# Kernel tuning notes

Hardware: AMD Instinct MI355X
Metric: run time of the kernel (lower is better)

Reference implementation:

```python
import jax, jax.numpy as jnp
import numpy as np

N, K, E = 20000, 4, 320000
IN_DIM, H_IN, D = 1024, 256, 128
GATE_IN = 2 * D + 1  # [h || m || logdeg]
GATE_H = 128         # max(d_out, 32)
TEMP = 0.6
M_CLAMP = 20.0


def _init(key, shape, fan_in):
    return jax.random.normal(key, shape, dtype=jnp.float32) / np.sqrt(fan_in)


def setup_inputs() -> dict:
    key = jax.random.key(0)
    ks = jax.random.split(key, 24)
    inp = {}
    inp['X'] = jax.random.normal(ks[0], (N, IN_DIM), dtype=jnp.float32)
    inp['rows'] = jax.random.randint(ks[1], (K, E), 0, N, dtype=jnp.int32)
    inp['cols'] = jax.random.randint(ks[2], (K, E), 0, N, dtype=jnp.int32)
    inp['mask'] = jnp.ones((N, K), dtype=jnp.float32)
    inp['logdeg'] = jax.random.uniform(ks[3], (N, K), dtype=jnp.float32) * 3.0
    # lin_in: 3-layer MLP 1024 -> 256 -> 256 -> 128, each + ReLU
    inp['W_in0'] = _init(ks[4], (IN_DIM, H_IN), IN_DIM); inp['b_in0'] = jnp.zeros((H_IN,), jnp.float32)
    inp['W_in1'] = _init(ks[5], (H_IN, H_IN), H_IN);     inp['b_in1'] = jnp.zeros((H_IN,), jnp.float32)
    inp['W_in2'] = _init(ks[6], (H_IN, D), H_IN);        inp['b_in2'] = jnp.zeros((D,), jnp.float32)
    # block 0
    inp['Wmsg0'] = _init(ks[7], (D, D), D)
    inp['Wg1_0'] = _init(ks[8], (GATE_IN, GATE_H), GATE_IN); inp['bg1_0'] = jnp.zeros((GATE_H,), jnp.float32)
    inp['Wg2_0'] = _init(ks[9], (GATE_H, 1), GATE_H);        inp['bg2_0'] = jnp.zeros((1,), jnp.float32)
    # block 1
    inp['Wmsg1'] = _init(ks[10], (D, D), D)
    inp['Wg1_1'] = _init(ks[11], (GATE_IN, GATE_H), GATE_IN); inp['bg1_1'] = jnp.zeros((GATE_H,), jnp.float32)
    inp['Wg2_1'] = _init(ks[12], (GATE_H, 1), GATE_H);        inp['bg2_1'] = jnp.zeros((1,), jnp.float32)
    # head
    inp['Wh1'] = _init(ks[13], (D, D), D); inp['bh1'] = jnp.zeros((D,), jnp.float32)
    inp['Wh2'] = _init(ks[14], (D, 1), D); inp['bh2'] = jnp.zeros((1,), jnp.float32)
    return inp


def reference(X, rows, cols, mask, logdeg,
              W_in0, b_in0, W_in1, b_in1, W_in2, b_in2,
              Wmsg0, Wg1_0, bg1_0, Wg2_0, bg2_0,
              Wmsg1, Wg1_1, bg1_1, Wg2_1, bg2_1,
              Wh1, bh1, Wh2, bh2):
    relu = jax.nn.relu
    # input encoder (eval mode: dropout / featdrop are identity)
    H = relu(relu(relu(X @ W_in0 + b_in0) @ W_in1 + b_in1) @ W_in2 + b_in2)

    def pairnorm(x):
        x = x - x.mean(axis=0, keepdims=True)
        mean_norm = jnp.sqrt(jnp.mean(jnp.sum(x * x, axis=1))) + 1e-6
        return x / mean_norm

    def block(H, Wmsg, Wg1, bg1, Wg2, bg2):
        Z = H @ Wmsg  # [N, D]
        def prop(r, c):  # sparse A_k @ Z with binary adjacency: out[r] += Z[c]
            return jax.ops.segment_sum(Z[c], r, num_segments=N)
        M = jnp.transpose(jax.vmap(prop)(rows, cols), (1, 0, 2))  # [N, K, D]
        M = jnp.clip(M, -M_CLAMP, M_CLAMP)
        H_rep = jnp.broadcast_to(H[:, None, :], (N, K, H.shape[1]))
        gate_in = jnp.concatenate([H_rep, M, logdeg[:, :, None]], axis=2)  # [N, K, 2D+1]
        scores = (relu(gate_in @ Wg1 + bg1) @ Wg2 + bg2)[..., 0]  # [N, K]
        alpha = jax.nn.softmax(scores / TEMP, axis=1)
        alpha = alpha * mask
        alpha = alpha / jnp.maximum(alpha.sum(axis=1, keepdims=True), 1e-12)
        alpha = jnp.maximum(alpha, 1e-8)
        alpha = alpha / jnp.maximum(alpha.sum(axis=1, keepdims=True), 1e-12)
        fused = jnp.einsum('nk,nkd->nd', alpha, M)
        return fused, alpha

    fused0, a0 = block(H, Wmsg0, Wg1_0, bg1_0, Wg2_0, bg2_0)
    H = relu(pairnorm(fused0 + H))
    fused1, a1 = block(H, Wmsg1, Wg1_1, bg1_1, Wg2_1, bg2_1)
    H = relu(pairnorm(fused1 + H))

    h = relu(relu(H) @ Wh1 + bh1)
    logits = (h @ Wh2 + bh2)[:, 0]  # [N]
    return logits, jnp.stack([a0, a1], axis=0)
```

## Files before the change

### kernel.cpp

```cpp
#include <hip/hip_runtime.h>
#include <hip/hip_bf16.h>

#define N_NODES 20000
#define KADJ 4
#define NEDGE 320000
#define ETOTAL (KADJ * NEDGE)
#define IN_DIM_ 1024
#define H_IN_ 256
#define DDIM 128
#define GATE_H_ 128
#define TEMP_ 0.6f
#define M_CLAMP_ 20.0f
#define CSR_TOTAL (KADJ * N_NODES)
#define NCOARSE 128
#define QPER (CSR_TOTAL / NCOARSE)
#define ESTRIDE 12288
#define TILE_A 4096
#define BINA_NB ((ETOTAL + TILE_A - 1) / TILE_A)
#define NB_CAST (N_NODES * IN_DIM_ / 8 / 256)
#define NB_TRANS 2560

typedef __attribute__((ext_vector_type(8))) short frag_ab;
typedef __attribute__((ext_vector_type(4))) float frag_cd;
typedef __attribute__((ext_vector_type(8))) unsigned short us8;

__device__ inline unsigned short f2bf(float f) {
    unsigned int u = __float_as_uint(f);
    u += 0x7FFFu + ((u >> 16) & 1);
    return (unsigned short)(u >> 16);
}
__device__ inline float bflo(unsigned int p) { return __uint_as_float(p << 16); }
__device__ inline float bfhi(unsigned int p) { return __uint_as_float(p & 0xffff0000u); }

__device__ __forceinline__ void gld16(const unsigned short* g, unsigned short* l) {
    __builtin_amdgcn_global_load_lds(
        (const __attribute__((address_space(1))) void*)g,
        (__attribute__((address_space(3))) void*)l, 16, 0, 0);
}

#define PIPE_WAIT_NEXT()  asm volatile("s_waitcnt vmcnt(5)" ::: "memory")
#define PIPE_WAIT_LAST()  asm volatile("s_waitcnt vmcnt(0)" ::: "memory")
#define PIPE_BAR()        __builtin_amdgcn_s_barrier()
#define PIPE_FENCE()      __builtin_amdgcn_sched_barrier(0)


struct TD { const float* src; unsigned short* dst; int K; int N; };
struct TD10 { TD d[10]; };

__global__ __launch_bounds__(256) void prep_kernel(
    const float* __restrict__ X, unsigned short* __restrict__ Xb,
    TD10 descs,
    const int* __restrict__ rows, const int* __restrict__ cols,
    int* __restrict__ bcnt, uint2* __restrict__ staging)
{
    __shared__ __align__(16) char sraw[2048 + TILE_A * 8];
    int bid = blockIdx.x;
    int tid = threadIdx.x;

    if (bid >= BINA_NB + NB_TRANS) {
        int i = ((bid - BINA_NB - NB_TRANS) * 256 + tid) * 8;
        float4 a = *(const float4*)(X + i), b = *(const float4*)(X + i + 4);
        us8 o;
        o[0] = f2bf(a.x); o[1] = f2bf(a.y); o[2] = f2bf(a.z); o[3] = f2bf(a.w);
        o[4] = f2bf(b.x); o[5] = f2bf(b.y); o[6] = f2bf(b.z); o[7] = f2bf(b.w);
        *(us8*)(Xb + i) = o;
        return;
    }
    if (bid >= BINA_NB) {
        int b2 = bid - BINA_NB;
        TD t = descs.d[b2 >> 8];
        int rem = b2 & 255;
        int n0 = (rem & 7) * 32, k0 = (rem >> 3) * 32;
        if (n0 >= t.N || k0 >= t.K) return;
        float (*tile)[33] = (float(*)[33])sraw;
        int tx = tid & 31, ty4 = (tid >> 5) * 4;
#pragma unroll
        for (int i = 0; i < 4; i++)
            tile[ty4 + i][tx] = t.src[(size_t)(k0 + ty4 + i) * t.N + n0 + tx];
        __syncthreads();
#pragma unroll
        for (int i = 0; i < 4; i++)
            t.dst[(size_t)(n0 + ty4 + i) * t.K + k0 + tx] = f2bf(tile[tx][ty4 + i]);
        return;
    }
    int* hist  = (int*)sraw;
    int* hscan = hist + NCOARSE;
    int* lcur  = hscan + NCOARSE;
    int* gbase = lcur + NCOARSE;
    uint2* pairs = (uint2*)(sraw + 2048);

    int base = bid * TILE_A;
    int cnt_t = min(TILE_A, ETOTAL - base);

    for (int i = tid; i < NCOARSE; i += 256) hist[i] = 0;
    __syncthreads();

    unsigned int q[16], c[16];
    bool valid[16];
#pragma unroll
    for (int i = 0; i < 16; i++) {
        int loc = i * 256 + tid;
        valid[i] = loc < cnt_t;
        if (valid[i]) {
            int e = base + loc;
            int k = e / NEDGE;
            unsigned int qq = (unsigned int)(k * N_NODES + rows[e]);
            q[i] = qq;
            c[i] = (unsigned int)cols[e];
            atomicAdd(&hist[qq / QPER], 1);
        }
    }
    __syncthreads();
    if (tid < NCOARSE) hscan[tid] = hist[tid];
    __syncthreads();
    for (int d = 1; d < NCOARSE; d <<= 1) {
        int v = (tid >= d && tid < NCOARSE) ? hscan[tid - d] : 0;
        __syncthreads();
        if (tid < NCOARSE) hscan[tid] += v;
        __syncthreads();
    }
    if (tid < NCOARSE) {
        int ex = hscan[tid] - hist[tid];
        hscan[tid] = ex;
        lcur[tid] = ex;
        gbase[tid] = hist[tid] ? (tid * ESTRIDE + atomicAdd(&bcnt[tid], hist[tid])) : 0;
    }
    __syncthreads();
#pragma unroll
    for (int i = 0; i < 16; i++) {
        if (valid[i]) {
            int b = q[i] / QPER;
            int p = atomicAdd(&lcur[b], 1);
            pairs[p] = make_uint2(q[i], c[i]);
        }
    }
    __syncthreads();
    for (int i = tid; i < cnt_t; i += 256) {
        uint2 pr = pairs[i];
        int b = pr.x / QPER;
        staging[gbase[b] + (i - hscan[b])] = pr;
    }
}

__global__ __launch_bounds__(256) void gemm1_binb_kernel(
    const unsigned short* __restrict__ A, const unsigned short* __restrict__ Bt,
    const float* __restrict__ bias, unsigned short* __restrict__ Cb,
    int M, int N, int K,
    const uint2* __restrict__ staging, const int* __restrict__ bcnt,
    int* __restrict__ offs, int* __restrict__ ends, int* __restrict__ edst)
{
    __shared__ __align__(16) char smem[40960];
    int tid = threadIdx.x;
    int bid = blockIdx.x;
    const int GEMM_NB = 2 * 625;

    if (bid < GEMM_NB) {
        unsigned short* sA0 = (unsigned short*)smem;
        unsigned short* sB0 = (unsigned short*)(smem + 8192);
        int tileM = (bid >> 1) * 32, tileN = (bid & 1) * 128;
        int w = tid >> 6, lane = tid & 63;
        int wr = (w & 1) * 16, wc = (w >> 1) * 64;
        int fm = lane & 15, fq = lane >> 4;
        int crow = lane >> 3;
        int gsw = (lane & 7) ^ crow;

        frag_cd acc[4] = {};

        auto stage = [&](int buf, int k0) {
            {
                int row = w * 8 + crow;
                int ar = min(tileM + row, M - 1);
                gld16(A + (size_t)ar * K + k0 + gsw * 8, sA0 + buf * 2048 + w * 512);
            }
#pragma unroll
            for (int t = 0; t < 4; t++) {
                int chunk = w * 4 + t;
                int row = chunk * 8 + crow;
                gld16(Bt + (size_t)(tileN + row) * K + k0 + gsw * 8, sB0 + buf * 8192 + chunk * 512);
            }
        };

        int nt = K >> 6;
        stage(0, 0);
        for (int t = 0; t < nt; t++) {
            int cur = t & 1;
            if (t + 1 < nt) { stage(cur ^ 1, (t + 1) << 6); PIPE_WAIT_NEXT(); }
            else            { PIPE_WAIT_LAST(); }
            PIPE_BAR();
            PIPE_FENCE();
#pragma unroll
            for (int s = 0; s < 2; s++) {
                int sw = ((s * 4 + fq) ^ (fm & 7)) * 8;
                frag_ab af = *(const frag_ab*)(sA0 + cur * 2048 + (wr + fm) * 64 + sw);
#pragma unroll
                for (int j = 0; j < 4; j++) {
                    frag_ab bf = *(const frag_ab*)(sB0 + cur * 8192 + (wc + j * 16 + fm) * 64 + sw);
                    acc[j] = __builtin_amdgcn_mfma_f32_16x16x32_bf16(af, bf, acc[j], 0, 0, 0);
                }
            }
            PIPE_FENCE();
            PIPE_BAR();
        }
        int row = tileM + wr + fq * 4;
#pragma unroll
        for (int r = 0; r < 4; r++) {
            if (row + r < M) {
#pragma unroll
                for (int j = 0; j < 4; j++) {
                    int col = tileN + wc + j * 16 + fm;
                    float v = fmaxf(acc[j][r] + bias[col], 0.f);
                    Cb[(size_t)(row + r) * N + col] = f2bf(v);
                }
            }
        }
        return;
    }
    int* cntS = (int*)smem;
    int* sofs = cntS + QPER;
    int* lcur = sofs + QPER;
    int* psum = lcur + QPER;
    int b = bid - GEMM_NB;
    int q0 = b * QPER, base = b * ESTRIDE;
    int fill = bcnt[b];
    for (int i = tid; i < QPER; i += 256) cntS[i] = 0;
    __syncthreads();
    for (int i = tid; i < fill; i += 256)
        atomicAdd(&cntS[staging[base + i].x - q0], 1);
    __syncthreads();
    const int CH = 3;
    int lo = tid * CH, hi = min(lo + CH, QPER);
    int s = 0;
    for (int i = lo; i < hi; i++) s += cntS[i];
    psum[tid] = s;
    __syncthreads();
    for (int d = 1; d < 256; d <<= 1) {
        int v = (tid >= d) ? psum[tid - d] : 0;
        __syncthreads();
        psum[tid] += v;
        __syncthreads();
    }
    int run = (tid == 0) ? 0 : psum[tid - 1];
    for (int i = lo; i < hi; i++) {
        sofs[i] = run;
        lcur[i] = run;
        run += cntS[i];
    }
    __syncthreads();
    for (int i = tid; i < QPER; i += 256) {
        offs[q0 + i] = base + sofs[i];
        ends[q0 + i] = base + sofs[i] + cntS[i];
    }
    for (int i = tid; i < fill; i += 256) {
        uint2 p = staging[base + i];
        int pos = atomicAdd(&lcur[p.x - q0], 1);
        edst[base + pos] = (int)p.y;
    }
}

__global__ __launch_bounds__(256) void gemm_async_kernel(
    const unsigned short* __restrict__ A, const unsigned short* __restrict__ Bt,
    const float* __restrict__ bias, float* __restrict__ Cf, unsigned short* __restrict__ Cb,
    int M, int N, int K, int do_relu)
{
    __shared__ unsigned short sA[2][32 * 64];
    __shared__ unsigned short sB[2][128 * 64];
    int tid = threadIdx.x;
    int tileM = blockIdx.y * 32, tileN = blockIdx.x * 128;
    int w = tid >> 6, lane = tid & 63;
    int wr = (w & 1) * 16, wc = (w >> 1) * 64;
    int fm = lane & 15, fq = lane >> 4;
    int crow = lane >> 3;
    int gsw = (lane & 7) ^ crow;

    frag_cd acc[4] = {};

    auto stage = [&](int buf, int k0) {
        {
            int row = w * 8 + crow;
            int ar = min(tileM + row, M - 1);
            gld16(A + (size_t)ar * K + k0 + gsw * 8, &sA[buf][w * 512]);
        }
#pragma unroll
        for (int t = 0; t < 4; t++) {
            int chunk = w * 4 + t;
            int row = chunk * 8 + crow;
            gld16(Bt + (size_t)(tileN + row) * K + k0 + gsw * 8, &sB[buf][chunk * 512]);
        }
    };

    int nt = K >> 6;
    stage(0, 0);
    for (int t = 0; t < nt; t++) {
        int cur = t & 1;
        if (t + 1 < nt) { stage(cur ^ 1, (t + 1) << 6); PIPE_WAIT_NEXT(); }
        else            { PIPE_WAIT_LAST(); }
        PIPE_BAR();
        PIPE_FENCE();
#pragma unroll
        for (int s = 0; s < 2; s++) {
            int sw = ((s * 4 + fq) ^ (fm & 7)) * 8;
            frag_ab af = *(const frag_ab*)&sA[cur][(wr + fm) * 64 + sw];
#pragma unroll
            for (int j = 0; j < 4; j++) {
                frag_ab bf = *(const frag_ab*)&sB[cur][(wc + j * 16 + fm) * 64 + sw];
                acc[j] = __builtin_amdgcn_mfma_f32_16x16x32_bf16(af, bf, acc[j], 0, 0, 0);
            }
        }
        PIPE_FENCE();
        PIPE_BAR();
    }
    int row = tileM + wr + fq * 4;
#pragma unroll
    for (int r = 0; r < 4; r++) {
        if (row + r < M) {
#pragma unroll
            for (int j = 0; j < 4; j++) {
                int col = tileN + wc + j * 16 + fm;
                float v = acc[j][r];
                if (bias) v += bias[col];
                if (do_relu) v = fmaxf(v, 0.f);
                if (Cf) Cf[(size_t)(row + r) * N + col] = v;
                if (Cb) Cb[(size_t)(row + r) * N + col] = f2bf(v);
            }
        }
    }
}

__global__ __launch_bounds__(256) void zg_gemm_kernel(
    const unsigned short* __restrict__ A, const unsigned short* __restrict__ Bt,
    const float* __restrict__ bg1, unsigned short* __restrict__ Zb,
    float* __restrict__ GH, int M)
{
    __shared__ unsigned short sA[2][32 * 64];
    __shared__ unsigned short sB[2][128 * 64];
    int tid = threadIdx.x;
    int tileM = blockIdx.y * 32, tileN = blockIdx.x * 128;
    int w = tid >> 6, lane = tid & 63;
    int wr = (w & 1) * 16, wc = (w >> 1) * 64;
    int fm = lane & 15, fq = lane >> 4;
    int crow = lane >> 3;
    int gsw = (lane & 7) ^ crow;

    frag_cd acc[4] = {};

    auto stage = [&](int buf, int k0) {
        {
            int row = w * 8 + crow;
            int ar = min(tileM + row, M - 1);
            gld16(A + (size_t)ar * DDIM + k0 + gsw * 8, &sA[buf][w * 512]);
        }
#pragma unroll
        for (int t = 0; t < 4; t++) {
            int chunk = w * 4 + t;
            int row = chunk * 8 + crow;
            gld16(Bt + (size_t)(tileN + row) * DDIM + k0 + gsw * 8, &sB[buf][chunk * 512]);
        }
    };

    stage(0, 0);
#pragma unroll
    for (int t = 0; t < 2; t++) {
        int cur = t & 1;
        if (t == 0) { stage(1, 64); PIPE_WAIT_NEXT(); }
        else        { PIPE_WAIT_LAST(); }
        PIPE_BAR();
        PIPE_FENCE();
#pragma unroll
        for (int s = 0; s < 2; s++) {
            int sw = ((s * 4 + fq) ^ (fm & 7)) * 8;
            frag_ab af = *(const frag_ab*)&sA[cur][(wr + fm) * 64 + sw];
#pragma unroll
            for (int j = 0; j < 4; j++) {
                frag_ab bf = *(const frag_ab*)&sB[cur][(wc + j * 16 + fm) * 64 + sw];
                acc[j] = __builtin_amdgcn_mfma_f32_16x16x32_bf16(af, bf, acc[j], 0, 0, 0);
            }
        }
        PIPE_FENCE();
        PIPE_BAR();
    }
    int isZ = (blockIdx.x == 0);
    int row = tileM + wr + fq * 4;
#pragma unroll
    for (int r = 0; r < 4; r++) {
        if (row + r < M) {
#pragma unroll
            for (int j = 0; j < 4; j++) {
                int col = wc + j * 16 + fm;
                float v = acc[j][r];
                if (isZ) Zb[(size_t)(row + r) * DDIM + col] = f2bf(v);
                else     GH[(size_t)(row + r) * GATE_H_ + col] = v + bg1[col];
            }
        }
    }
}

__global__ __launch_bounds__(256) void head_gemm_kernel(
    const unsigned short* __restrict__ A, const unsigned short* __restrict__ Bt,
    const float* __restrict__ bh1, const float* __restrict__ Wh2,
    const float* __restrict__ bh2, float* __restrict__ logits, int M)
{
    __shared__ unsigned short sA[2][32 * 64];
    __shared__ unsigned short sB[2][128 * 64];
    __shared__ float sred[2][32];
    int tid = threadIdx.x;
    int tileM = blockIdx.x * 32;
    int w = tid >> 6, lane = tid & 63;
    int wr = (w & 1) * 16, wc = (w >> 1) * 64;
    int fm = lane & 15, fq = lane >> 4;
    int crow = lane >> 3;
    int gsw = (lane & 7) ^ crow;

    frag_cd acc[4] = {};

    auto stage = [&](int buf, int k0) {
        {
            int row = w * 8 + crow;
            int ar = min(tileM + row, M - 1);
            gld16(A + (size_t)ar * DDIM + k0 + gsw * 8, &sA[buf][w * 512]);
        }
#pragma unroll
        for (int t = 0; t < 4; t++) {
            int chunk = w * 4 + t;
            int row = chunk * 8 + crow;
            gld16(Bt + (size_t)row * DDIM + k0 + gsw * 8, &sB[buf][chunk * 512]);
        }
    };

    stage(0, 0);
#pragma unroll
    for (int t = 0; t < 2; t++) {
        int cur = t & 1;
        if (t == 0) { stage(1, 64); PIPE_WAIT_NEXT(); }
        else        { PIPE_WAIT_LAST(); }
        PIPE_BAR();
        PIPE_FENCE();
#pragma unroll
        for (int s = 0; s < 2; s++) {
            int sw = ((s * 4 + fq) ^ (fm & 7)) * 8;
            frag_ab af = *(const frag_ab*)&sA[cur][(wr + fm) * 64 + sw];
#pragma unroll
            for (int j = 0; j < 4; j++) {
                frag_ab bf = *(const frag_ab*)&sB[cur][(wc + j * 16 + fm) * 64 + sw];
                acc[j] = __builtin_amdgcn_mfma_f32_16x16x32_bf16(af, bf, acc[j], 0, 0, 0);
            }
        }
        PIPE_FENCE();
        PIPE_BAR();
    }
    float wv[4], bh[4];
#pragma unroll
    for (int j = 0; j < 4; j++) {
        int c = wc + j * 16 + fm;
        wv[j] = Wh2[c];
        bh[j] = bh1[c];
    }
    float part[4];
#pragma unroll
    for (int r = 0; r < 4; r++) {
        float p = 0.f;
#pragma unroll
        for (int j = 0; j < 4; j++) {
            float v = fmaxf(acc[j][r] + bh[j], 0.f);
            p += v * wv[j];
        }
        part[r] = p;
    }
#pragma unroll
    for (int m = 1; m < 16; m <<= 1)
#pragma unroll
        for (int r = 0; r < 4; r++)
            part[r] += __shfl_xor(part[r], m, 64);
    if (fm == 0) {
#pragma unroll
        for (int r = 0; r < 4; r++)
            sred[w >> 1][wr + fq * 4 + r] = part[r];
    }
    __syncthreads();
    if (tid < 32 && tileM + tid < M)
        logits[tileM + tid] = sred[0][tid] + sred[1][tid] + bh2[0];
}

__global__ __launch_bounds__(256) void gate_fuse_kernel(
    const int* __restrict__ offs, const int* __restrict__ ends,
    const int* __restrict__ edst, const unsigned short* __restrict__ Zb,
    const unsigned short* __restrict__ Bt,
    const float* __restrict__ GH, const float* __restrict__ logdeg,
    const float* __restrict__ wld, const float* __restrict__ Wg2,
    const float* __restrict__ bg2, const float* __restrict__ mask,
    const float* __restrict__ H, float* __restrict__ Y,
    float* __restrict__ alpha_out, float* __restrict__ red)
{
    __shared__ __align__(16) unsigned short sA[2][32 * 64];
    __shared__ __align__(16) unsigned short sB[2][128 * 64];
    __shared__ float sred[2][32];
    __shared__ float sc_al[64];
    __shared__ float sx[256], sy[256], sqs[256];
    int tid = threadIdx.x;
    int tile0 = blockIdx.x * 32;
    int node0 = blockIdx.x * 8;
    int w = tid >> 6, lane = tid & 63;
    int wr = (w & 1) * 16, wc = (w >> 1) * 64;
    int fm = lane & 15, fq = lane >> 4;
    int crow = lane >> 3;
    int gsw = (lane & 7) ^ crow;

#pragma unroll
    for (int t = 0; t < 4; t++) {
        int chunk = w * 4 + t;
        int row = chunk * 8 + crow;
        gld16(Bt + (size_t)row * DDIM + 0  + gsw * 8, &sB[0][chunk * 512]);
        gld16(Bt + (size_t)row * DDIM + 64 + gsw * 8, &sB[1][chunk * 512]);
    }

    int qw = lane >> 4;
    int l = lane & 15;
    for (int qi = 0; qi < 8; qi++) {
        int lq = w * 8 + qi;
        int qp = tile0 + lq;
        int r = qp >> 2, kk = qp & 3;
        int qc = kk * N_NODES + r;
        int start = offs[qc], end = ends[qc];

        float a0 = 0.f, a1 = 0.f, a2 = 0.f, a3 = 0.f;
        float a4 = 0.f, a5 = 0.f, a6 = 0.f, a7 = 0.f;
#define ACC8(P) {                                  \
        a0 += bflo(P.x); a1 += bfhi(P.x);          \
        a2 += bflo(P.y); a3 += bfhi(P.y);          \
        a4 += bflo(P.z); a5 += bfhi(P.z);          \
        a6 += bflo(P.w); a7 += bfhi(P.w); }
        int i = start + qw;
        for (; i + 12 < end; i += 16) {
            int c0 = edst[i], c1 = edst[i + 4], c2 = edst[i + 8], c3 = edst[i + 12];
            uint4 p0 = *(const uint4*)(Zb + (size_t)c0 * DDIM + l * 8);
            uint4 p1 = *(const uint4*)(Zb + (size_t)c1 * DDIM + l * 8);
            uint4 p2 = *(const uint4*)(Zb + (size_t)c2 * DDIM + l * 8);
            uint4 p3 = *(const uint4*)(Zb + (size_t)c3 * DDIM + l * 8);
            ACC8(p0); ACC8(p1); ACC8(p2); ACC8(p3);
        }
        for (; i + 4 < end; i += 8) {
            int c0 = edst[i], c1 = edst[i + 4];
            uint4 p0 = *(const uint4*)(Zb + (size_t)c0 * DDIM + l * 8);
            uint4 p1 = *(const uint4*)(Zb + (size_t)c1 * DDIM + l * 8);
            ACC8(p0); ACC8(p1);
        }
        if (i < end) {
            int c0 = edst[i];
            uint4 p0 = *(const uint4*)(Zb + (size_t)c0 * DDIM + l * 8);
            ACC8(p0);
        }
#undef ACC8
#define QRED(x) { x += __shfl_xor(x, 16, 64); x += __shfl_xor(x, 32, 64); }
        QRED(a0) QRED(a1) QRED(a2) QRED(a3) QRED(a4) QRED(a5) QRED(a6) QRED(a7)
#undef QRED
        if (qw == 0) {
#define CLIP(v) fminf(fmaxf(v, -M_CLAMP_), M_CLAMP_)
            unsigned int w0 = (unsigned int)f2bf(CLIP(a0)) | ((unsigned int)f2bf(CLIP(a1)) << 16);
            unsigned int w1 = (unsigned int)f2bf(CLIP(a2)) | ((unsigned int)f2bf(CLIP(a3)) << 16);
            unsigned int w2 = (unsigned int)f2bf(CLIP(a4)) | ((unsigned int)f2bf(CLIP(a5)) << 16);
            unsigned int w3 = (unsigned int)f2bf(CLIP(a6)) | ((unsigned int)f2bf(CLIP(a7)) << 16);
#undef CLIP
            int buf = l >> 3, gg = l & 7, cr = lq & 7;
            int soff = w * 512 + (cr * 8 + (gg ^ cr)) * 8;
            *(uint4*)&sA[buf][soff] = make_uint4(w0, w1, w2, w3);
        }
    }
    __syncthreads();

    frag_cd acc[4] = {};
#pragma unroll
    for (int tkt = 0; tkt < 2; tkt++) {
#pragma unroll
        for (int s = 0; s < 2; s++) {
            int sw = ((s * 4 + fq) ^ (fm & 7)) * 8;
            frag_ab af = *(const frag_ab*)&sA[tkt][(wr + fm) * 64 + sw];
#pragma unroll
            for (int j = 0; j < 4; j++) {
                frag_ab bf = *(const frag_ab*)&sB[tkt][(wc + j * 16 + fm) * 64 + sw];
                acc[j] = __builtin_amdgcn_mfma_f32_16x16x32_bf16(af, bf, acc[j], 0, 0, 0);
            }
        }
    }
    float wg2v[4], wldv[4];
#pragma unroll
    for (int j = 0; j < 4; j++) {
        int c = wc + j * 16 + fm;
        wg2v[j] = Wg2[c];
        wldv[j] = wld[c];
    }
    float part[4];
#pragma unroll
    for (int r = 0; r < 4; r++) {
        int q = tile0 + wr + fq * 4 + r;
        int n = q >> 2;
        float ld = logdeg[q];
        float p = 0.f;
#pragma unroll
        for (int j = 0; j < 4; j++) {
            int c = wc + j * 16 + fm;
            float v = acc[j][r] + GH[(size_t)n * GATE_H_ + c] + ld * wldv[j];
            p += fmaxf(v, 0.f) * wg2v[j];
        }
        part[r] = p;
    }
#pragma unroll
    for (int m = 1; m < 16; m <<= 1)
#pragma unroll
        for (int r = 0; r < 4; r++)
            part[r] += __shfl_xor(part[r], m, 64);
    if (fm == 0) {
#pragma unroll
        for (int r = 0; r < 4; r++)
            sred[w >> 1][wr + fq * 4 + r] = part[r];
    }
    __syncthreads();
    if (tid < 32) sc_al[tid] = sred[0][tid] + sred[1][tid] + bg2[0];
    __syncthreads();
    if (tid < 8) {
        int n = node0 + tid;
        float a[KADJ];
        float mx = -1e30f;
#pragma unroll
        for (int k = 0; k < KADJ; k++) {
            a[k] = sc_al[tid * 4 + k] * (1.0f / TEMP_);
            mx = fmaxf(mx, a[k]);
        }
        float sum = 0.f;
#pragma unroll
        for (int k = 0; k < KADJ; k++) { a[k] = expf(a[k] - mx); sum += a[k]; }
#pragma unroll
        for (int k = 0; k < KADJ; k++) a[k] = (a[k] / sum) * mask[(size_t)n * KADJ + k];
        float s2 = 0.f;
#pragma unroll
        for (int k = 0; k < KADJ; k++) s2 += a[k];
        float inv = 1.f / fmaxf(s2, 1e-12f);
#pragma unroll
        for (int k = 0; k < KADJ; k++) a[k] = fmaxf(a[k] * inv, 1e-8f);
        s2 = 0.f;
#pragma unroll
        for (int k = 0; k < KADJ; k++) s2 += a[k];
        inv = 1.f / fmaxf(s2, 1e-12f);
#pragma unroll
        for (int k = 0; k < KADJ; k++) sc_al[32 + tid * 4 + k] = a[k] * inv;
    }
    __syncthreads();
    if (tid < 32) alpha_out[tile0 + tid] = sc_al[32 + tid];
    float csx = 0.f, csy = 0.f, sq = 0.f;
    int j = tid & 63, dd = j * 2;
    int g = dd >> 3, mbuf = g >> 3, gg2 = g & 7, din = dd & 7;
#pragma unroll
    for (int it = 0; it < 2; it++) {
        int nl = (tid >> 6) + it * 4;
        int n = node0 + nl;
        const float* alp = &sc_al[32 + nl * 4];
        float2 h = *(const float2*)(H + (size_t)n * DDIM + dd);
        float yx = h.x, yy = h.y;
#pragma unroll
        for (int k = 0; k < KADJ; k++) {
            int row = nl * 4 + k;
            int soff = (row >> 3) * 512 + ((row & 7) * 8 + (gg2 ^ (row & 7))) * 8 + din;
            unsigned int u = *(const unsigned int*)&sA[mbuf][soff];
            yx += alp[k] * bflo(u);
            yy += alp[k] * bfhi(u);
        }
        *(float2*)(Y + (size_t)n * DDIM + dd) = make_float2(yx, yy);
        csx += yx; csy += yy;
        sq += yx * yx + yy * yy;
    }
    sx[tid] = csx; sy[tid] = csy; sqs[tid] = sq;
    __syncthreads();
    int st = (blockIdx.x & 7) * 132;
    if (tid < 64) {
        float ax = sx[tid] + sx[tid + 64] + sx[tid + 128] + sx[tid + 192];
        float ay = sy[tid] + sy[tid + 64] + sy[tid + 128] + sy[tid + 192];
        atomicAdd(&red[st + tid * 2], ax);
        atomicAdd(&red[st + tid * 2 + 1], ay);
    }
    for (int s = 128; s > 0; s >>= 1) {
        if (tid < s) sqs[tid] += sqs[tid + s];
        __syncthreads();
    }
    if (tid == 0) atomicAdd(&red[st + 128], sqs[0]);
}

__global__ __launch_bounds__(256) void pairnorm_kernel(
    const float* __restrict__ Y, const float* __restrict__ red,
    float* __restrict__ Hout, unsigned short* __restrict__ Hb, int N)
{
    int tid = threadIdx.x;
    int d = tid & 127;
    float invN = 1.0f / (float)N;
    float s = 0.f, rq = 0.f;
#pragma unroll
    for (int st = 0; st < 8; st++) {
        s += red[st * 132 + d];
        rq += red[st * 132 + 128];
    }
    float mu = s * invN;
    __shared__ float smu2[128];
    if (tid < 128) smu2[tid] = mu * mu;
    __syncthreads();
    for (int t = 64; t > 0; t >>= 1) {
        if (tid < t) smu2[tid] += smu2[tid + t];
        __syncthreads();
    }
    float summu2 = smu2[0];
    float var = rq * invN - summu2;
    float norm = sqrtf(fmaxf(var, 0.f)) + 1e-6f;
    float inv = 1.0f / norm;
    int n = blockIdx.x * 2 + (tid >> 7);
    if (n < N) {
        float v = (Y[(size_t)n * DDIM + d] - mu) * inv;
        v = fmaxf(v, 0.f);
        Hout[(size_t)n * DDIM + d] = v;
        Hb[(size_t)n * DDIM + d] = f2bf(v);
    }
}

extern "C" void kernel_launch(void* const* d_in, const int* in_sizes, int n_in,
                              void* d_out, int out_size, void* d_ws, size_t ws_size,
                              hipStream_t stream)
{
    const float* X      = (const float*)d_in[0];
    const int*   rows   = (const int*)d_in[1];
    const int*   cols   = (const int*)d_in[2];
    const float* mask   = (const float*)d_in[3];
    const float* logdeg = (const float*)d_in[4];
    const float* W_in0  = (const float*)d_in[5];
    const float* b_in0  = (const float*)d_in[6];
    const float* W_in1  = (const float*)d_in[7];
    const float* b_in1  = (const float*)d_in[8];
    const float* W_in2  = (const float*)d_in[9];
    const float* b_in2  = (const float*)d_in[10];
    const float* Wmsg[2] = {(const float*)d_in[11], (const float*)d_in[16]};
    const float* Wg1[2]  = {(const float*)d_in[12], (const float*)d_in[17]};
    const float* bg1[2]  = {(const float*)d_in[13], (const float*)d_in[18]};
    const float* Wg2[2]  = {(const float*)d_in[14], (const float*)d_in[19]};
    const float* bg2[2]  = {(const float*)d_in[15], (const float*)d_in[20]};
    const float* Wh1 = (const float*)d_in[21];
    const float* bh1 = (const float*)d_in[22];
    const float* Wh2 = (const float*)d_in[23];
    const float* bh2 = (const float*)d_in[24];

    float* ws = (float*)d_ws;
    unsigned short* Xb  = (unsigned short*)ws;
    float* Ybuf  = ws + 5120000;
    float* GH    = ws + 7680000;
    unsigned short* H0b = (unsigned short*)(ws + 10240000);
    unsigned short* H1b = (unsigned short*)(ws + 12800000);
    unsigned short* Zb  = (unsigned short*)(ws + 12800000);
    uint2* staging = (uint2*)(ws + 15360000);
    float* H     = ws + 15360000;
    unsigned short* Hb = (unsigned short*)(ws + 17920000);
    int*   bcnt  = (int*)(ws + 19200000);
    float* red   = ws + 19200128;
    int*   offs   = (int*)(ws + 19280000);
    int*   ends   = (int*)(ws + 19360000);
    int*   edst   = (int*)(ws + 19440000);
    unsigned short* w0t  = (unsigned short*)(ws + 21013248);
    unsigned short* w1t  = (unsigned short*)(ws + 21144320);
    unsigned short* w2t  = (unsigned short*)(ws + 21177088);
    unsigned short* wzg[2]  = {(unsigned short*)(ws + 21193472), (unsigned short*)(ws + 21209856)};
    unsigned short* wgmt[2] = {(unsigned short*)(ws + 21226240), (unsigned short*)(ws + 21234432)};
    unsigned short* wh1t = (unsigned short*)(ws + 21242624);
    float* logits = (float*)d_out;
    float* alpha_out = (float*)d_out + N_NODES;

    dim3 blk(256);
    int gM32 = (N_NODES + 31) / 32;

    (void)hipMemsetAsync(bcnt, 0, (128 + 2 * 8 * 132) * sizeof(float), stream);

    TD10 descs;
    descs.d[0] = {W_in0, w0t, IN_DIM_, H_IN_};
    descs.d[1] = {W_in1, w1t, H_IN_, H_IN_};
    descs.d[2] = {W_in2, w2t, H_IN_, DDIM};
    descs.d[3] = {Wmsg[0], wzg[0], DDIM, DDIM};
    descs.d[4] = {Wg1[0], wzg[0] + DDIM * DDIM, DDIM, GATE_H_};
    descs.d[5] = {Wmsg[1], wzg[1], DDIM, DDIM};
    descs.d[6] = {Wg1[1], wzg[1] + DDIM * DDIM, DDIM, GATE_H_};
    descs.d[7] = {Wg1[0] + DDIM * GATE_H_, wgmt[0], DDIM, GATE_H_};
    descs.d[8] = {Wg1[1] + DDIM * GATE_H_, wgmt[1], DDIM, GATE_H_};
    descs.d[9] = {Wh1, wh1t, DDIM, DDIM};
    prep_kernel<<<BINA_NB + NB_TRANS + NB_CAST, blk, 0, stream>>>(
        X, Xb, descs, rows, cols, bcnt, staging);

    gemm1_binb_kernel<<<2 * gM32 + NCOARSE, blk, 0, stream>>>(
        Xb, w0t, b_in0, H0b, N_NODES, H_IN_, IN_DIM_,
        staging, bcnt, offs, ends, edst);

    gemm_async_kernel<<<dim3(2, gM32), blk, 0, stream>>>(H0b, w1t, b_in1, nullptr, H1b, N_NODES, H_IN_, H_IN_, 1);
    gemm_async_kernel<<<dim3(1, gM32), blk, 0, stream>>>(H1b, w2t, b_in2, H, Hb, N_NODES, DDIM, H_IN_, 1);

    for (int b = 0; b < 2; b++) {
        zg_gemm_kernel<<<dim3(2, gM32), blk, 0, stream>>>(Hb, wzg[b], bg1[b], Zb, GH, N_NODES);
        float* alph = alpha_out + (size_t)b * N_NODES * KADJ;
        gate_fuse_kernel<<<CSR_TOTAL / 32, blk, 0, stream>>>(
            offs, ends, edst, Zb, wgmt[b], GH, logdeg, Wg1[b] + 256 * GATE_H_,
            Wg2[b], bg2[b], mask, H, Ybuf, alph, red + b * 8 * 132);
        pairnorm_kernel<<<(N_NODES + 1) / 2, blk, 0, stream>>>(Ybuf, red + b * 8 * 132, H, Hb, N_NODES);
    }

    head_gemm_kernel<<<gM32, blk, 0, stream>>>(Hb, wh1t, bh1, Wh2, bh2, logits, N_NODES);
}
```

Before: 469.9 us.

## Split neighbor gather out of gate kernel into a wide parallel gather pass

Adds a dedicated gather kernel that sums neighbor Z rows for each (node, adjacency) pair. It launches one wave per pair and feature half, and writes the clipped bf16 messages M to a global buffer that aliases the dead Xb region. The gate/fuse kernel then streams M and the gate weights into LDS with double-buffered async loads, and reads M again from global for the alpha-weighted fusion. This removes the serial 8-queries-per-wave gather that limited parallelism in the fused kernel. The cost is an extra global write and read of M per block, plus one more launch.

```diff
diff --git a/kernel.cpp b/kernel.cpp
--- a/kernel.cpp
+++ b/kernel.cpp
@@ -43,7 +43,6 @@
 #define PIPE_BAR()        __builtin_amdgcn_s_barrier()
 #define PIPE_FENCE()      __builtin_amdgcn_sched_barrier(0)
 
-
 struct TD { const float* src; unsigned short* dst; int K; int N; };
 struct TD10 { TD d[10]; };
 
@@ -480,18 +479,74 @@
         logits[tileM + tid] = sred[0][tid] + sred[1][tid] + bh2[0];
 }
 
+__global__ __launch_bounds__(256) void gather_kernel(
+    const int* __restrict__ offs, const int* __restrict__ ends,
+    const int* __restrict__ edst,
+    const unsigned short* __restrict__ Zb, unsigned short* __restrict__ Mb)
+{
+    int bid = blockIdx.x;
+    int half = (bid >> 2) & 1;
+    int qgroup = (bid >> 3) * 4 + (bid & 3);
+    int w = threadIdx.x >> 6;
+    int q = qgroup * 4 + w;
+    int lane = threadIdx.x & 63;
+    int eg = lane >> 3;
+    int l = lane & 7;
+    int k = q / N_NODES;
+    int r = q - k * N_NODES;
+    int start = offs[q];
+    int end = ends[q];
+    const unsigned short* Zh = Zb + half * 64 + l * 8;
+
+    float a0 = 0.f, a1 = 0.f, a2 = 0.f, a3 = 0.f;
+    float a4 = 0.f, a5 = 0.f, a6 = 0.f, a7 = 0.f;
+
+#define ACC8(P) {                                  \
+        a0 += bflo(P.x); a1 += bfhi(P.x);          \
+        a2 += bflo(P.y); a3 += bfhi(P.y);          \
+        a4 += bflo(P.z); a5 += bfhi(P.z);          \
+        a6 += bflo(P.w); a7 += bfhi(P.w); }
+
+    int i = start + eg;
+    for (; i + 8 < end; i += 16) {
+        int c0 = edst[i], c1 = edst[i + 8];
+        uint4 p0 = *(const uint4*)(Zh + (size_t)c0 * DDIM);
+        uint4 p1 = *(const uint4*)(Zh + (size_t)c1 * DDIM);
+        ACC8(p0); ACC8(p1);
+    }
+    if (i < end) {
+        int c0 = edst[i];
+        uint4 p0 = *(const uint4*)(Zh + (size_t)c0 * DDIM);
+        ACC8(p0);
+    }
+#undef ACC8
+
+#define GRED(x) { x += __shfl_xor(x, 8, 64); x += __shfl_xor(x, 16, 64); x += __shfl_xor(x, 32, 64); }
+    GRED(a0) GRED(a1) GRED(a2) GRED(a3) GRED(a4) GRED(a5) GRED(a6) GRED(a7)
+#undef GRED
+
+#define CLIP(v) fminf(fmaxf(v, -M_CLAMP_), M_CLAMP_)
+    unsigned int w0 = (unsigned int)f2bf(CLIP(a0)) | ((unsigned int)f2bf(CLIP(a1)) << 16);
+    unsigned int w1 = (unsigned int)f2bf(CLIP(a2)) | ((unsigned int)f2bf(CLIP(a3)) << 16);
+    unsigned int w2 = (unsigned int)f2bf(CLIP(a4)) | ((unsigned int)f2bf(CLIP(a5)) << 16);
+    unsigned int w3 = (unsigned int)f2bf(CLIP(a6)) | ((unsigned int)f2bf(CLIP(a7)) << 16);
+#undef CLIP
+    if (eg == 0) {
+        uint4 o = make_uint4(w0, w1, w2, w3);
+        *(uint4*)(Mb + ((size_t)r * KADJ + k) * DDIM + half * 64 + l * 8) = o;
+    }
+}
+
 __global__ __launch_bounds__(256) void gate_fuse_kernel(
-    const int* __restrict__ offs, const int* __restrict__ ends,
-    const int* __restrict__ edst, const unsigned short* __restrict__ Zb,
-    const unsigned short* __restrict__ Bt,
+    const unsigned short* __restrict__ Mb, const unsigned short* __restrict__ Bt,
     const float* __restrict__ GH, const float* __restrict__ logdeg,
     const float* __restrict__ wld, const float* __restrict__ Wg2,
     const float* __restrict__ bg2, const float* __restrict__ mask,
     const float* __restrict__ H, float* __restrict__ Y,
     float* __restrict__ alpha_out, float* __restrict__ red)
 {
-    __shared__ __align__(16) unsigned short sA[2][32 * 64];
-    __shared__ __align__(16) unsigned short sB[2][128 * 64];
+    __shared__ unsigned short sA[2][32 * 64];
+    __shared__ unsigned short sB[2][128 * 64];
     __shared__ float sred[2][32];
     __shared__ float sc_al[64];
     __shared__ float sx[256], sy[256], sqs[256];
@@ -504,81 +559,41 @@
     int crow = lane >> 3;
     int gsw = (lane & 7) ^ crow;
 
-#pragma unroll
-    for (int t = 0; t < 4; t++) {
-        int chunk = w * 4 + t;
-        int row = chunk * 8 + crow;
-        gld16(Bt + (size_t)row * DDIM + 0  + gsw * 8, &sB[0][chunk * 512]);
-        gld16(Bt + (size_t)row * DDIM + 64 + gsw * 8, &sB[1][chunk * 512]);
-    }
-
-    int qw = lane >> 4;
-    int l = lane & 15;
-    for (int qi = 0; qi < 8; qi++) {
-        int lq = w * 8 + qi;
-        int qp = tile0 + lq;
-        int r = qp >> 2, kk = qp & 3;
-        int qc = kk * N_NODES + r;
-        int start = offs[qc], end = ends[qc];
-
-        float a0 = 0.f, a1 = 0.f, a2 = 0.f, a3 = 0.f;
-        float a4 = 0.f, a5 = 0.f, a6 = 0.f, a7 = 0.f;
-#define ACC8(P) {                                  \
-        a0 += bflo(P.x); a1 += bfhi(P.x);          \
-        a2 += bflo(P.y); a3 += bfhi(P.y);          \
-        a4 += bflo(P.z); a5 += bfhi(P.z);          \
-        a6 += bflo(P.w); a7 += bfhi(P.w); }
-        int i = start + qw;
-        for (; i + 12 < end; i += 16) {
-            int c0 = edst[i], c1 = edst[i + 4], c2 = edst[i + 8], c3 = edst[i + 12];
-            uint4 p0 = *(const uint4*)(Zb + (size_t)c0 * DDIM + l * 8);
-            uint4 p1 = *(const uint4*)(Zb + (size_t)c1 * DDIM + l * 8);
-            uint4 p2 = *(const uint4*)(Zb + (size_t)c2 * DDIM + l * 8);
-            uint4 p3 = *(const uint4*)(Zb + (size_t)c3 * DDIM + l * 8);
-            ACC8(p0); ACC8(p1); ACC8(p2); ACC8(p3);
-        }
-        for (; i + 4 < end; i += 8) {
-            int c0 = edst[i], c1 = edst[i + 4];
-            uint4 p0 = *(const uint4*)(Zb + (size_t)c0 * DDIM + l * 8);
-            uint4 p1 = *(const uint4*)(Zb + (size_t)c1 * DDIM + l * 8);
-            ACC8(p0); ACC8(p1);
-        }
-        if (i < end) {
-            int c0 = edst[i];
-            uint4 p0 = *(const uint4*)(Zb + (size_t)c0 * DDIM + l * 8);
-            ACC8(p0);
-        }
-#undef ACC8
-#define QRED(x) { x += __shfl_xor(x, 16, 64); x += __shfl_xor(x, 32, 64); }
-        QRED(a0) QRED(a1) QRED(a2) QRED(a3) QRED(a4) QRED(a5) QRED(a6) QRED(a7)
-#undef QRED
-        if (qw == 0) {
-#define CLIP(v) fminf(fmaxf(v, -M_CLAMP_), M_CLAMP_)
-            unsigned int w0 = (unsigned int)f2bf(CLIP(a0)) | ((unsigned int)f2bf(CLIP(a1)) << 16);
-            unsigned int w1 = (unsigned int)f2bf(CLIP(a2)) | ((unsigned int)f2bf(CLIP(a3)) << 16);
-            unsigned int w2 = (unsigned int)f2bf(CLIP(a4)) | ((unsigned int)f2bf(CLIP(a5)) << 16);
-            unsigned int w3 = (unsigned int)f2bf(CLIP(a6)) | ((unsigned int)f2bf(CLIP(a7)) << 16);
-#undef CLIP
-            int buf = l >> 3, gg = l & 7, cr = lq & 7;
-            int soff = w * 512 + (cr * 8 + (gg ^ cr)) * 8;
-            *(uint4*)&sA[buf][soff] = make_uint4(w0, w1, w2, w3);
-        }
-    }
-    __syncthreads();
-
     frag_cd acc[4] = {};
-#pragma unroll
-    for (int tkt = 0; tkt < 2; tkt++) {
+
+    auto stage = [&](int buf, int k0) {
+        {
+            int row = w * 8 + crow;
+            gld16(Mb + (size_t)(tile0 + row) * DDIM + k0 + gsw * 8, &sA[buf][w * 512]);
+        }
+#pragma unroll
+        for (int t = 0; t < 4; t++) {
+            int chunk = w * 4 + t;
+            int row = chunk * 8 + crow;
+            gld16(Bt + (size_t)row * DDIM + k0 + gsw * 8, &sB[buf][chunk * 512]);
+        }
+    };
+
+    stage(0, 0);
+#pragma unroll
+    for (int t = 0; t < 2; t++) {
+        int cur = t & 1;
+        if (t == 0) { stage(1, 64); PIPE_WAIT_NEXT(); }
+        else        { PIPE_WAIT_LAST(); }
+        PIPE_BAR();
+        PIPE_FENCE();
 #pragma unroll
         for (int s = 0; s < 2; s++) {
             int sw = ((s * 4 + fq) ^ (fm & 7)) * 8;
-            frag_ab af = *(const frag_ab*)&sA[tkt][(wr + fm) * 64 + sw];
+            frag_ab af = *(const frag_ab*)&sA[cur][(wr + fm) * 64 + sw];
 #pragma unroll
             for (int j = 0; j < 4; j++) {
-                frag_ab bf = *(const frag_ab*)&sB[tkt][(wc + j * 16 + fm) * 64 + sw];
+                frag_ab bf = *(const frag_ab*)&sB[cur][(wc + j * 16 + fm) * 64 + sw];
                 acc[j] = __builtin_amdgcn_mfma_f32_16x16x32_bf16(af, bf, acc[j], 0, 0, 0);
             }
         }
+        PIPE_FENCE();
+        PIPE_BAR();
     }
     float wg2v[4], wldv[4];
 #pragma unroll
@@ -646,7 +661,6 @@
     if (tid < 32) alpha_out[tile0 + tid] = sc_al[32 + tid];
     float csx = 0.f, csy = 0.f, sq = 0.f;
     int j = tid & 63, dd = j * 2;
-    int g = dd >> 3, mbuf = g >> 3, gg2 = g & 7, din = dd & 7;
 #pragma unroll
     for (int it = 0; it < 2; it++) {
         int nl = (tid >> 6) + it * 4;
@@ -656,9 +670,7 @@
         float yx = h.x, yy = h.y;
 #pragma unroll
         for (int k = 0; k < KADJ; k++) {
-            int row = nl * 4 + k;
-            int soff = (row >> 3) * 512 + ((row & 7) * 8 + (gg2 ^ (row & 7))) * 8 + din;
-            unsigned int u = *(const unsigned int*)&sA[mbuf][soff];
+            unsigned int u = *(const unsigned int*)(Mb + ((size_t)n * KADJ + k) * DDIM + dd);
             yx += alp[k] * bflo(u);
             yy += alp[k] * bfhi(u);
         }
@@ -743,6 +755,7 @@
 
     float* ws = (float*)d_ws;
     unsigned short* Xb  = (unsigned short*)ws;
+    unsigned short* Mb  = (unsigned short*)ws;
     float* Ybuf  = ws + 5120000;
     float* GH    = ws + 7680000;
     unsigned short* H0b = (unsigned short*)(ws + 10240000);
@@ -793,10 +806,11 @@
 
     for (int b = 0; b < 2; b++) {
         zg_gemm_kernel<<<dim3(2, gM32), blk, 0, stream>>>(Hb, wzg[b], bg1[b], Zb, GH, N_NODES);
+        gather_kernel<<<CSR_TOTAL / 2, blk, 0, stream>>>(offs, ends, edst, Zb, Mb);
         float* alph = alpha_out + (size_t)b * N_NODES * KADJ;
         gate_fuse_kernel<<<CSR_TOTAL / 32, blk, 0, stream>>>(
-            offs, ends, edst, Zb, wgmt[b], GH, logdeg, Wg1[b] + 256 * GATE_H_,
-            Wg2[b], bg2[b], mask, H, Ybuf, alph, red + b * 8 * 132);
+            Mb, wgmt[b], GH, logdeg, Wg1[b] + 256 * GATE_H_, Wg2[b], bg2[b],
+            mask, H, Ybuf, alph, red + b * 8 * 132);
         pairnorm_kernel<<<(N_NODES + 1) / 2, blk, 0, stream>>>(Ybuf, red + b * 8 * 132, H, Hb, N_NODES);
     }
 
```

Result: no change. 463.3 us (-1.4%).
